# Performance work log

Measured on AMD Instinct MI355X. Metric: run time of the kernel, lower is better.

## Reference

```python
import jax, jax.numpy as jnp
import numpy as np

EPS_LN = 1e-5
EPS_D = 1e-8
K = 3

def layer_norm(x, g, b):
    mu = jnp.mean(x, axis=-1, keepdims=True)
    var = jnp.var(x, axis=-1, keepdims=True)
    return (x - mu) * jax.lax.rsqrt(var + EPS_LN) * g + b

def setup_inputs() -> dict:
    key = jax.random.key(0)
    ks = jax.random.split(key, 8)
    Nc, Nu, Cin, Cout = 4096, 16384, 256, 256
    return {
        "x_feat": jax.random.normal(ks[0], (Nc, Cin), jnp.float32),
        "x_pos": jax.random.uniform(ks[1], (Nc, 3), jnp.float32),
        "xup_feat": jax.random.normal(ks[2], (Nu, Cout), jnp.float32),
        "xup_pos": jax.random.uniform(ks[3], (Nu, 3), jnp.float32),
        "g1": jnp.ones((Cin,), jnp.float32),
        "b1": jnp.zeros((Cin,), jnp.float32),
        "W": jax.random.normal(ks[4], (Cin, Cout), jnp.float32) * 0.02,
        "b": jnp.zeros((Cout,), jnp.float32),
        "g2": jnp.ones((Cout,), jnp.float32),
        "b2": jnp.zeros((Cout,), jnp.float32),
        "W_up": jax.random.normal(ks[5], (Cout, Cout), jnp.float32) * 0.02,
        "b_up": jnp.zeros((Cout,), jnp.float32),
    }

def reference(x_feat, x_pos, xup_feat, xup_pos, g1, b1, W, b, g2, b2, W_up, b_up):
    # norm -> linear on coarse points: [Nc, Cout]
    x = layer_norm(x_feat, g1, b1) @ W + b
    # norm -> linear on fine points:   [Nu, Cout]
    xu = layer_norm(xup_feat, g2, b2) @ W_up + b_up
    # squared pairwise distances fine->coarse: [Nu, Nc]
    d2 = (jnp.sum(xup_pos * xup_pos, axis=-1, keepdims=True)
          - 2.0 * (xup_pos @ x_pos.T)
          + jnp.sum(x_pos * x_pos, axis=-1))
    # k nearest coarse neighbors per fine point
    neg_d2, idx = jax.lax.top_k(-d2, K)          # [Nu, K]
    w = 1.0 / (-neg_d2 + EPS_D)                  # inverse-distance weights
    w = w / jnp.sum(w, axis=-1, keepdims=True)
    # gather + weighted sum: [Nu, Cout]
    interp = jnp.einsum('uk,ukc->uc', w, x[idx])
    return interp + xu
```

## Files before the change

kernel.cpp:

```cpp
#include <hip/hip_runtime.h>

#define EPS_LN 1e-5f
#define EPS_D  1e-8f
#define BIGD 3.402823466e+38f

typedef __attribute__((ext_vector_type(8))) short s16x8;
typedef __attribute__((ext_vector_type(4))) float f32x4;
typedef __attribute__((ext_vector_type(4))) unsigned short u16x4;

#define XC_OFF    0u
#define XH_OFF    4194304u
#define XL_OFF    14680064u
#define MU_OFF    25165824u
#define RS_OFF    25247744u
#define WGH_OFF   25329664u
#define WGL_OFF   25460736u
#define WUGH_OFF  25591808u
#define WUGL_OFF  25722880u
#define C12_OFF   25853952u
#define CPS_OFF   25858048u
#define IDXS_OFF  25923584u
#define CST_OFF   25939968u
#define UPS_OFF   25944064u
#define USORT_OFF 26206208u

__device__ __forceinline__ int cell_of(float px, float py, float pz) {
    int cx = (int)(px * 8.0f); cx = cx < 0 ? 0 : (cx > 7 ? 7 : cx);
    int cy = (int)(py * 8.0f); cy = cy < 0 ? 0 : (cy > 7 ? 7 : cy);
    int cz = (int)(pz * 8.0f); cz = cz < 0 ? 0 : (cz > 7 ? 7 : cz);
    return (cz * 8 + cy) * 8 + cx;
}

__global__ __launch_bounds__(1024) void prep_kernel(
    const float* __restrict__ x_feat, const float* __restrict__ xup_feat,
    const float* __restrict__ x_pos, const float* __restrict__ xup_pos,
    const float* __restrict__ W, const float* __restrict__ W_up,
    const float* __restrict__ g1, const float* __restrict__ b1,
    const float* __restrict__ g2, const float* __restrict__ b2,
    float* __restrict__ mu, float* __restrict__ rs,
    unsigned short* __restrict__ xh, unsigned short* __restrict__ xl,
    unsigned short* __restrict__ wgh, unsigned short* __restrict__ wgl,
    unsigned short* __restrict__ wugh, unsigned short* __restrict__ wugl,
    float* __restrict__ c12,
    float4* __restrict__ cps, int* __restrict__ idxs, int* __restrict__ cellStart,
    float4* __restrict__ ups, int* __restrict__ usort)
{
    __shared__ float smemf[2048];
    int* const cnt   = (int*)smemf;
    int* const ofs   = ((int*)smemf) + 512;
    __shared__ int wpart[8];
    __shared__ int wpref[8];

    const int bid = blockIdx.x, tid = threadIdx.x;
    const int lane = tid & 63, wave = tid >> 6;

    if (bid < 2) {
        const bool fine = (bid == 0);
        const int npts = fine ? 16384 : 4096;
        const float* pos = fine ? xup_pos : x_pos;

        if (tid < 512) cnt[tid] = 0;
        __syncthreads();
        for (int i = tid; i < npts; i += 1024) {
            const int c = cell_of(pos[i*3+0], pos[i*3+1], pos[i*3+2]);
            atomicAdd(&cnt[c], 1);
        }
        __syncthreads();
        int v = 0, incl = 0;
        if (wave < 8) {
            const int cell = wave * 64 + lane;
            v = cnt[cell];
            incl = v;
            #pragma unroll
            for (int off = 1; off < 64; off <<= 1) {
                const int t = __shfl_up(incl, off);
                if (lane >= off) incl += t;
            }
            if (lane == 63) wpart[wave] = incl;
        }
        __syncthreads();
        if (tid == 0) {
            int run = 0;
            #pragma unroll
            for (int w = 0; w < 8; ++w) { wpref[w] = run; run += wpart[w]; }
        }
        __syncthreads();
        if (wave < 8) {
            const int cell = wave * 64 + lane;
            const int excl = incl - v + wpref[wave];
            ofs[cell] = excl;
            if (!fine) cellStart[cell] = excl;
        }
        if (!fine && tid == 0) cellStart[512] = 4096;
        __syncthreads();
        for (int i = tid; i < npts; i += 1024) {
            const float px = pos[i*3+0], py = pos[i*3+1], pz = pos[i*3+2];
            const int c = cell_of(px, py, pz);
            const int slot = atomicAdd(&ofs[c], 1);
            if (fine) {
                ups[slot] = make_float4(px, py, pz, px*px + py*py + pz*pz);
                usort[slot] = i;
            } else {
                cps[slot] = make_float4(px, py, pz, px*px + py*py + pz*pz);
                idxs[slot] = i;
            }
        }
    } else if (bid < 4) {
        const bool fine = (bid == 2);
        const float* src = fine ? W_up : W;
        const float* g   = fine ? g2 : g1;
        const float* bln = fine ? b2 : b1;
        float* c1 = c12 + (fine ? 0 : 512);
        float* c2 = c12 + (fine ? 256 : 768);
        const int col = tid & 255, kg = tid >> 8;
        float a1 = 0.0f, a2 = 0.0f;
        for (int k = kg * 64; k < kg * 64 + 64; ++k) {
            const float wv = src[(size_t)k * 256 + col];
            a1 = fmaf(bln[k], wv, a1);
            a2 = fmaf(g[k],   wv, a2);
        }
        smemf[kg * 256 + col] = a1;
        smemf[1024 + kg * 256 + col] = a2;
        __syncthreads();
        if (kg == 0) {
            c1[col] = smemf[col] + smemf[256 + col] + smemf[512 + col] + smemf[768 + col];
            c2[col] = smemf[1024 + col] + smemf[1280 + col] + smemf[1536 + col] + smemf[1792 + col];
        }
    } else if (bid < 8) {
        const int mb = (bid - 4) * 4 + (tid >> 8);
        const int t = tid & 255;
        const float* src = (mb < 8) ? W : W_up;
        const float* g   = (mb < 8) ? g1 : g2;
        unsigned short* dh = (mb < 8) ? wgh : wugh;
        unsigned short* dl = (mb < 8) ? wgl : wugl;
        const int n  = (mb & 7) * 32 + (t >> 3);
        const int kc = (t & 7) * 32;
        for (int kk = 0; kk < 32; kk += 4) {
            u16x4 hv, lv;
            #pragma unroll
            for (int c = 0; c < 4; ++c) {
                const int k = kc + kk + c;
                const float wv = g[k] * src[(size_t)k * 256 + n];
                const unsigned ua = __float_as_uint(wv);
                hv[c] = (unsigned short)(ua >> 16);
                const float lo = wv - __uint_as_float(ua & 0xFFFF0000u);
                lv[c] = (unsigned short)(__float_as_uint(lo) >> 16);
            }
            *(u16x4*)&dh[(size_t)n * 256 + kc + kk] = hv;
            *(u16x4*)&dl[(size_t)n * 256 + kc + kk] = lv;
        }
    } else {
        const int rbase = (bid - 8) * 128 + wave * 8;
        #pragma unroll
        for (int rr = 0; rr < 8; ++rr) {
            const int r = rbase + rr;
            const float* src = (r < 16384) ? (xup_feat + (size_t)r * 256)
                                           : (x_feat + (size_t)(r - 16384) * 256);
            const float4 v = ((const float4*)src)[lane];
            float s  = v.x + v.y + v.z + v.w;
            float ss = v.x*v.x + v.y*v.y + v.z*v.z + v.w*v.w;
            #pragma unroll
            for (int off = 1; off < 64; off <<= 1) {
                s  += __shfl_xor(s,  off);
                ss += __shfl_xor(ss, off);
            }
            if (lane == 0) {
                const float m   = s * (1.0f / 256.0f);
                const float var = ss * (1.0f / 256.0f) - m * m;
                mu[r] = m;
                rs[r] = rsqrtf(var + EPS_LN);
            }
            const float vv[4] = { v.x, v.y, v.z, v.w };
            u16x4 hv, lv;
            #pragma unroll
            for (int c = 0; c < 4; ++c) {
                const unsigned ua = __float_as_uint(vv[c]);
                hv[c] = (unsigned short)(ua >> 16);
                const float lo = vv[c] - __uint_as_float(ua & 0xFFFF0000u);
                lv[c] = (unsigned short)(__float_as_uint(lo) >> 16);
            }
            *(u16x4*)&xh[(size_t)r * 256 + lane * 4] = hv;
            *(u16x4*)&xl[(size_t)r * 256 + lane * 4] = lv;
        }
    }
}

__global__ __launch_bounds__(256) void gemm_kernel(
    const unsigned short* __restrict__ xh, const unsigned short* __restrict__ xl,
    const float* __restrict__ mu, const float* __restrict__ rs,
    const unsigned short* __restrict__ wgh, const unsigned short* __restrict__ wgl,
    const unsigned short* __restrict__ wugh, const unsigned short* __restrict__ wugl,
    const float* __restrict__ c12,
    const float* __restrict__ b_up, const float* __restrict__ bb,
    float* __restrict__ outF, float* __restrict__ outC)
{
    const int bid = blockIdx.x;
    const unsigned short *BH, *BL; const float *c1, *c2, *bias; float* OUT;
    int row0, col0, statbase;
    if (bid < 256) {
        BH = wugh; BL = wugl; c1 = c12; c2 = c12 + 256; bias = b_up; OUT = outF;
        row0 = (bid >> 1) * 128; col0 = (bid & 1) * 128; statbase = 0;
    } else {
        const int id = bid - 256;
        BH = wgh; BL = wgl; c1 = c12 + 512; c2 = c12 + 768; bias = bb; OUT = outC;
        row0 = (id >> 1) * 128; col0 = (id & 1) * 128; statbase = 16384;
    }

    const int lane = threadIdx.x & 63;
    const int wave = threadIdx.x >> 6;
    const int wr = wave >> 1, wc = wave & 1;
    const int lm = lane & 15, lk = lane >> 4;

    int arow[4];
    #pragma unroll
    for (int mf = 0; mf < 4; ++mf)
        arow[mf] = statbase + row0 + wr * 64 + mf * 16 + lm;

    int ncol[4]; float c1v[4], c2v[4], bv[4];
    #pragma unroll
    for (int nf = 0; nf < 4; ++nf) {
        ncol[nf] = col0 + wc * 64 + nf * 16 + lm;
        c1v[nf] = c1[ncol[nf]];
        c2v[nf] = c2[ncol[nf]];
        bv[nf]  = bias[ncol[nf]];
    }

    f32x4 acc[4][4];
    #pragma unroll
    for (int mf = 0; mf < 4; ++mf)
        #pragma unroll
        for (int nf = 0; nf < 4; ++nf)
            acc[mf][nf] = (f32x4){0.0f, 0.0f, 0.0f, 0.0f};

    for (int k0 = 0; k0 < 256; k0 += 32) {
        const int kb = k0 + lk * 8;

        s16x8 bh[4], bl[4], ah[4], al[4];
        #pragma unroll
        for (int nf = 0; nf < 4; ++nf) {
            const size_t o = (size_t)ncol[nf] * 256 + kb;
            bh[nf] = *(const s16x8*)(BH + o);
            bl[nf] = *(const s16x8*)(BL + o);
        }
        #pragma unroll
        for (int mf = 0; mf < 4; ++mf) {
            const size_t o = (size_t)arow[mf] * 256 + kb;
            ah[mf] = *(const s16x8*)(xh + o);
            al[mf] = *(const s16x8*)(xl + o);
        }

        #pragma unroll
        for (int mf = 0; mf < 4; ++mf)
            #pragma unroll
            for (int nf = 0; nf < 4; ++nf) {
                acc[mf][nf] = __builtin_amdgcn_mfma_f32_16x16x32_bf16(ah[mf], bh[nf], acc[mf][nf], 0, 0, 0);
                acc[mf][nf] = __builtin_amdgcn_mfma_f32_16x16x32_bf16(ah[mf], bl[nf], acc[mf][nf], 0, 0, 0);
                acc[mf][nf] = __builtin_amdgcn_mfma_f32_16x16x32_bf16(al[mf], bh[nf], acc[mf][nf], 0, 0, 0);
            }
    }

    #pragma unroll
    for (int mf = 0; mf < 4; ++mf) {
        #pragma unroll
        for (int q = 0; q < 4; ++q) {
            const int orow = row0 + wr * 64 + mf * 16 + lk * 4 + q;
            const float m = mu[statbase + orow];
            const float s = rs[statbase + orow];
            const float ms = -m * s;
            #pragma unroll
            for (int nf = 0; nf < 4; ++nf)
                OUT[(size_t)orow * 256 + ncol[nf]] =
                    fmaf(s, acc[mf][nf][q], fmaf(ms, c2v[nf], c1v[nf]) + bv[nf]);
        }
    }
}

__device__ __forceinline__ void ins3(float d, int p,
    float& b0, float& b1, float& b2, int& p0, int& p1, int& p2)
{
    const bool lt0 = d < b0, lt1 = d < b1, lt2 = d < b2;
    const float n1 = lt0 ? b0 : (lt1 ? d : b1);
    const int   q1 = lt0 ? p0 : (lt1 ? p : p1);
    const float n2 = lt1 ? b1 : (lt2 ? d : b2);
    const int   q2 = lt1 ? p1 : (lt2 ? p : p2);
    b0 = lt0 ? d : b0;  p0 = lt0 ? p : p0;
    b1 = n1; p1 = q1;
    b2 = n2; p2 = q2;
}

__global__ __launch_bounds__(256) void topk_kernel(
    const float4* __restrict__ cps, const int* __restrict__ idxs,
    const int* __restrict__ cellStart,
    const float4* __restrict__ ups, const int* __restrict__ usort,
    const float* __restrict__ xc, float* __restrict__ out)
{
    __shared__ float pd[4][64][3];
    __shared__ int   pp[4][64][3];
    __shared__ float wsel[64][3];
    __shared__ int   isel[64][3];
    __shared__ int   uor[64];
    __shared__ int   cst[513];

    const int tid = threadIdx.x, lane = tid & 63, wave = tid >> 6;
    const int su = blockIdx.x * 64 + lane;

    for (int i = tid; i < 513; i += 256) cst[i] = cellStart[i];

    const float4 up = ups[su];
    const float ux = up.x, uy = up.y, uz = up.z, uu = up.w;
    if (wave == 0) uor[lane] = usort[su];
    int cx = (int)(ux * 8.0f); cx = cx < 0 ? 0 : (cx > 7 ? 7 : cx);
    int cy = (int)(uy * 8.0f); cy = cy < 0 ? 0 : (cy > 7 ? 7 : cy);
    int cz = (int)(uz * 8.0f); cz = cz < 0 ? 0 : (cz > 7 ? 7 : cz);

    __syncthreads();

    float b0 = BIGD, b1 = BIGD, b2 = BIGD;
    int p0 = 0, p1 = 0, p2 = 0;

    for (int cc = wave; cc < 27; cc += 4) {
        const int nx = cx + (cc % 3) - 1;
        const int ny = cy + ((cc / 3) % 3) - 1;
        const int nz = cz + (cc / 9) - 1;
        if ((unsigned)nx > 7u || (unsigned)ny > 7u || (unsigned)nz > 7u) continue;
        const int cell = (nz * 8 + ny) * 8 + nx;
        const int s = cst[cell], e = cst[cell + 1];
        if (s >= e) continue;
        float4 c = cps[s];
        for (int p = s; p < e; ++p) {
            const float4 nxt = (p + 1 < e) ? cps[p + 1] : c;
            const float dot = ux * c.x + uy * c.y + uz * c.z;
            const float d = (uu - 2.0f * dot) + c.w;
            ins3(d, p, b0, b1, b2, p0, p1, p2);
            c = nxt;
        }
    }

    pd[wave][lane][0] = b0; pd[wave][lane][1] = b1; pd[wave][lane][2] = b2;
    pp[wave][lane][0] = p0; pp[wave][lane][1] = p1; pp[wave][lane][2] = p2;
    __syncthreads();

    if (wave == 0) {
        for (int w = 1; w < 4; ++w) {
            #pragma unroll
            for (int e = 0; e < 3; ++e)
                ins3(pd[w][lane][e], pp[w][lane][e], b0, b1, b2, p0, p1, p2);
        }

        const float h = 0.125f;
        float gmin = BIGD;
        if (cx > 0) gmin = fminf(gmin, ux - (float)(cx - 1) * h);
        if (cx < 7) gmin = fminf(gmin, (float)(cx + 2) * h - ux);
        if (cy > 0) gmin = fminf(gmin, uy - (float)(cy - 1) * h);
        if (cy < 7) gmin = fminf(gmin, (float)(cy + 2) * h - uy);
        if (cz > 0) gmin = fminf(gmin, uz - (float)(cz - 1) * h);
        if (cz < 7) gmin = fminf(gmin, (float)(cz + 2) * h - uz);

        if (b2 > gmin * gmin) {
            b0 = b1 = b2 = BIGD; p0 = p1 = p2 = 0;
            for (int p = 0; p < 4096; ++p) {
                const float4 c = cps[p];
                const float dot = ux * c.x + uy * c.y + uz * c.z;
                const float d = (uu - 2.0f * dot) + c.w;
                ins3(d, p, b0, b1, b2, p0, p1, p2);
            }
        }

        float w0 = 1.0f / (b0 + EPS_D);
        float w1 = 1.0f / (b1 + EPS_D);
        float w2 = 1.0f / (b2 + EPS_D);
        const float inv = 1.0f / (w0 + w1 + w2);
        wsel[lane][0] = w0 * inv; wsel[lane][1] = w1 * inv; wsel[lane][2] = w2 * inv;
        isel[lane][0] = idxs[p0]; isel[lane][1] = idxs[p1]; isel[lane][2] = idxs[p2];
    }
    __syncthreads();

    #pragma unroll
    for (int r = 0; r < 16; ++r) {
        const int ul = wave * 16 + r;
        const float w0 = wsel[ul][0], w1 = wsel[ul][1], w2 = wsel[ul][2];
        const int a0 = isel[ul][0], a1 = isel[ul][1], a2 = isel[ul][2];
        const float4 v0 = ((const float4*)(xc + (size_t)a0 * 256))[lane];
        const float4 v1 = ((const float4*)(xc + (size_t)a1 * 256))[lane];
        const float4 v2 = ((const float4*)(xc + (size_t)a2 * 256))[lane];
        float4* op = (float4*)(out + (size_t)uor[ul] * 256);
        float4 o = op[lane];
        o.x += w0 * v0.x + w1 * v1.x + w2 * v2.x;
        o.y += w0 * v0.y + w1 * v1.y + w2 * v2.y;
        o.z += w0 * v0.z + w1 * v1.z + w2 * v2.z;
        o.w += w0 * v0.w + w1 * v1.w + w2 * v2.w;
        op[lane] = o;
    }
}

extern "C" void kernel_launch(void* const* d_in, const int* in_sizes, int n_in,
                              void* d_out, int out_size, void* d_ws, size_t ws_size,
                              hipStream_t stream)
{
    const float* x_feat   = (const float*)d_in[0];
    const float* x_pos    = (const float*)d_in[1];
    const float* xup_feat = (const float*)d_in[2];
    const float* xup_pos  = (const float*)d_in[3];
    const float* g1       = (const float*)d_in[4];
    const float* b1       = (const float*)d_in[5];
    const float* W        = (const float*)d_in[6];
    const float* bb       = (const float*)d_in[7];
    const float* g2       = (const float*)d_in[8];
    const float* b2       = (const float*)d_in[9];
    const float* W_up     = (const float*)d_in[10];
    const float* b_up     = (const float*)d_in[11];

    float* out = (float*)d_out;
    char*  ws  = (char*)d_ws;

    float* xc  = (float*)(ws + XC_OFF);
    unsigned short* xh   = (unsigned short*)(ws + XH_OFF);
    unsigned short* xl   = (unsigned short*)(ws + XL_OFF);
    float* mu  = (float*)(ws + MU_OFF);
    float* rs  = (float*)(ws + RS_OFF);
    unsigned short* wgh  = (unsigned short*)(ws + WGH_OFF);
    unsigned short* wgl  = (unsigned short*)(ws + WGL_OFF);
    unsigned short* wugh = (unsigned short*)(ws + WUGH_OFF);
    unsigned short* wugl = (unsigned short*)(ws + WUGL_OFF);
    float* c12 = (float*)(ws + C12_OFF);
    float4* cps = (float4*)(ws + CPS_OFF);
    int* idxs   = (int*)(ws + IDXS_OFF);
    int* cstart = (int*)(ws + CST_OFF);
    float4* ups = (float4*)(ws + UPS_OFF);
    int* usort  = (int*)(ws + USORT_OFF);

    prep_kernel<<<168, 1024, 0, stream>>>(x_feat, xup_feat, x_pos, xup_pos,
                                          W, W_up, g1, b1, g2, b2,
                                          mu, rs, xh, xl,
                                          wgh, wgl, wugh, wugl,
                                          c12, cps, idxs, cstart, ups, usort);
    gemm_kernel<<<320, 256, 0, stream>>>(xh, xl, mu, rs,
                                         wgh, wgl, wugh, wugl,
                                         c12, b_up, bb, out, xc);
    topk_kernel<<<256, 256, 0, stream>>>(cps, idxs, cstart, ups, usort, xc, out);
}
```

Before: 180.5 us.

## Split prep and topk kernels; decouple kNN search from gather-interpolation

Splits the prep kernel into a small block for spatial-grid and weight prep and a streaming block for layer-norm stats and bf16 hi/lo splitting. Also splits the top-k kernel into a kNN kernel that writes weights and indices to workspace, and a separate interpolation kernel with more, smaller blocks. The kNN search now runs before the GEMM, so it no longer sits behind it. The cost is two extra launches, serialized on one stream, plus a round trip through global memory for the selected weights and indices.

```diff
diff --git a/kernel.cpp b/kernel.cpp
--- a/kernel.cpp
+++ b/kernel.cpp
@@ -23,6 +23,8 @@
 #define CST_OFF   25939968u
 #define UPS_OFF   25944064u
 #define USORT_OFF 26206208u
+#define WSEL_OFF  26271744u
+#define ISEL_OFF  26468352u
 
 __device__ __forceinline__ int cell_of(float px, float py, float pz) {
     int cx = (int)(px * 8.0f); cx = cx < 0 ? 0 : (cx > 7 ? 7 : cx);
@@ -31,14 +33,11 @@
     return (cz * 8 + cy) * 8 + cx;
 }
 
-__global__ __launch_bounds__(1024) void prep_kernel(
-    const float* __restrict__ x_feat, const float* __restrict__ xup_feat,
+__global__ __launch_bounds__(1024) void prep_small_kernel(
     const float* __restrict__ x_pos, const float* __restrict__ xup_pos,
     const float* __restrict__ W, const float* __restrict__ W_up,
     const float* __restrict__ g1, const float* __restrict__ b1,
     const float* __restrict__ g2, const float* __restrict__ b2,
-    float* __restrict__ mu, float* __restrict__ rs,
-    unsigned short* __restrict__ xh, unsigned short* __restrict__ xl,
     unsigned short* __restrict__ wgh, unsigned short* __restrict__ wgl,
     unsigned short* __restrict__ wugh, unsigned short* __restrict__ wugl,
     float* __restrict__ c12,
@@ -46,8 +45,8 @@
     float4* __restrict__ ups, int* __restrict__ usort)
 {
     __shared__ float smemf[2048];
-    int* const cnt   = (int*)smemf;
-    int* const ofs   = ((int*)smemf) + 512;
+    int* const cnt = (int*)smemf;
+    int* const ofs = ((int*)smemf) + 512;
     __shared__ int wpart[8];
     __shared__ int wpref[8];
 
@@ -126,7 +125,7 @@
             c1[col] = smemf[col] + smemf[256 + col] + smemf[512 + col] + smemf[768 + col];
             c2[col] = smemf[1024 + col] + smemf[1280 + col] + smemf[1536 + col] + smemf[1792 + col];
         }
-    } else if (bid < 8) {
+    } else {
         const int mb = (bid - 4) * 4 + (tid >> 8);
         const int t = tid & 255;
         const float* src = (mb < 8) ? W : W_up;
@@ -149,39 +148,46 @@
             *(u16x4*)&dh[(size_t)n * 256 + kc + kk] = hv;
             *(u16x4*)&dl[(size_t)n * 256 + kc + kk] = lv;
         }
-    } else {
-        const int rbase = (bid - 8) * 128 + wave * 8;
-        #pragma unroll
-        for (int rr = 0; rr < 8; ++rr) {
-            const int r = rbase + rr;
-            const float* src = (r < 16384) ? (xup_feat + (size_t)r * 256)
-                                           : (x_feat + (size_t)(r - 16384) * 256);
-            const float4 v = ((const float4*)src)[lane];
-            float s  = v.x + v.y + v.z + v.w;
-            float ss = v.x*v.x + v.y*v.y + v.z*v.z + v.w*v.w;
-            #pragma unroll
-            for (int off = 1; off < 64; off <<= 1) {
-                s  += __shfl_xor(s,  off);
-                ss += __shfl_xor(ss, off);
-            }
-            if (lane == 0) {
-                const float m   = s * (1.0f / 256.0f);
-                const float var = ss * (1.0f / 256.0f) - m * m;
-                mu[r] = m;
-                rs[r] = rsqrtf(var + EPS_LN);
-            }
-            const float vv[4] = { v.x, v.y, v.z, v.w };
-            u16x4 hv, lv;
-            #pragma unroll
-            for (int c = 0; c < 4; ++c) {
-                const unsigned ua = __float_as_uint(vv[c]);
-                hv[c] = (unsigned short)(ua >> 16);
-                const float lo = vv[c] - __uint_as_float(ua & 0xFFFF0000u);
-                lv[c] = (unsigned short)(__float_as_uint(lo) >> 16);
-            }
-            *(u16x4*)&xh[(size_t)r * 256 + lane * 4] = hv;
-            *(u16x4*)&xl[(size_t)r * 256 + lane * 4] = lv;
-        }
+    }
+}
+
+__global__ __launch_bounds__(1024) void prep_stream_kernel(
+    const float* __restrict__ x_feat, const float* __restrict__ xup_feat,
+    float* __restrict__ mu, float* __restrict__ rs,
+    unsigned short* __restrict__ xh, unsigned short* __restrict__ xl)
+{
+    const int lane = threadIdx.x & 63, wave = threadIdx.x >> 6;
+    const int rbase = blockIdx.x * 128 + wave * 8;
+    #pragma unroll
+    for (int rr = 0; rr < 8; ++rr) {
+        const int r = rbase + rr;
+        const float* src = (r < 16384) ? (xup_feat + (size_t)r * 256)
+                                       : (x_feat + (size_t)(r - 16384) * 256);
+        const float4 v = ((const float4*)src)[lane];
+        float s  = v.x + v.y + v.z + v.w;
+        float ss = v.x*v.x + v.y*v.y + v.z*v.z + v.w*v.w;
+        #pragma unroll
+        for (int off = 1; off < 64; off <<= 1) {
+            s  += __shfl_xor(s,  off);
+            ss += __shfl_xor(ss, off);
+        }
+        if (lane == 0) {
+            const float m   = s * (1.0f / 256.0f);
+            const float var = ss * (1.0f / 256.0f) - m * m;
+            mu[r] = m;
+            rs[r] = rsqrtf(var + EPS_LN);
+        }
+        const float vv[4] = { v.x, v.y, v.z, v.w };
+        u16x4 hv, lv;
+        #pragma unroll
+        for (int c = 0; c < 4; ++c) {
+            const unsigned ua = __float_as_uint(vv[c]);
+            hv[c] = (unsigned short)(ua >> 16);
+            const float lo = vv[c] - __uint_as_float(ua & 0xFFFF0000u);
+            lv[c] = (unsigned short)(__float_as_uint(lo) >> 16);
+        }
+        *(u16x4*)&xh[(size_t)r * 256 + lane * 4] = hv;
+        *(u16x4*)&xl[(size_t)r * 256 + lane * 4] = lv;
     }
 }
 
@@ -288,17 +294,14 @@
     b2 = n2; p2 = q2;
 }
 
-__global__ __launch_bounds__(256) void topk_kernel(
+__global__ __launch_bounds__(256) void knn_kernel(
     const float4* __restrict__ cps, const int* __restrict__ idxs,
     const int* __restrict__ cellStart,
-    const float4* __restrict__ ups, const int* __restrict__ usort,
-    const float* __restrict__ xc, float* __restrict__ out)
+    const float4* __restrict__ ups,
+    float* __restrict__ wsel, int* __restrict__ isel)
 {
     __shared__ float pd[4][64][3];
     __shared__ int   pp[4][64][3];
-    __shared__ float wsel[64][3];
-    __shared__ int   isel[64][3];
-    __shared__ int   uor[64];
     __shared__ int   cst[513];
 
     const int tid = threadIdx.x, lane = tid & 63, wave = tid >> 6;
@@ -308,7 +311,6 @@
 
     const float4 up = ups[su];
     const float ux = up.x, uy = up.y, uz = up.z, uu = up.w;
-    if (wave == 0) uor[lane] = usort[su];
     int cx = (int)(ux * 8.0f); cx = cx < 0 ? 0 : (cx > 7 ? 7 : cx);
     int cy = (int)(uy * 8.0f); cy = cy < 0 ? 0 : (cy > 7 ? 7 : cy);
     int cz = (int)(uz * 8.0f); cz = cz < 0 ? 0 : (cz > 7 ? 7 : cz);
@@ -370,20 +372,27 @@
         float w1 = 1.0f / (b1 + EPS_D);
         float w2 = 1.0f / (b2 + EPS_D);
         const float inv = 1.0f / (w0 + w1 + w2);
-        wsel[lane][0] = w0 * inv; wsel[lane][1] = w1 * inv; wsel[lane][2] = w2 * inv;
-        isel[lane][0] = idxs[p0]; isel[lane][1] = idxs[p1]; isel[lane][2] = idxs[p2];
-    }
-    __syncthreads();
-
-    #pragma unroll
-    for (int r = 0; r < 16; ++r) {
-        const int ul = wave * 16 + r;
-        const float w0 = wsel[ul][0], w1 = wsel[ul][1], w2 = wsel[ul][2];
-        const int a0 = isel[ul][0], a1 = isel[ul][1], a2 = isel[ul][2];
+        wsel[su*3+0] = w0 * inv; wsel[su*3+1] = w1 * inv; wsel[su*3+2] = w2 * inv;
+        isel[su*3+0] = idxs[p0]; isel[su*3+1] = idxs[p1]; isel[su*3+2] = idxs[p2];
+    }
+}
+
+__global__ __launch_bounds__(256) void interp_kernel(
+    const float* __restrict__ wsel, const int* __restrict__ isel,
+    const int* __restrict__ usort,
+    const float* __restrict__ xc, float* __restrict__ out)
+{
+    const int lane = threadIdx.x & 63, wave = threadIdx.x >> 6;
+    const int base = blockIdx.x * 32 + wave * 8;
+    #pragma unroll
+    for (int r = 0; r < 8; ++r) {
+        const int su = base + r;
+        const float w0 = wsel[su*3+0], w1 = wsel[su*3+1], w2 = wsel[su*3+2];
+        const int a0 = isel[su*3+0], a1 = isel[su*3+1], a2 = isel[su*3+2];
         const float4 v0 = ((const float4*)(xc + (size_t)a0 * 256))[lane];
         const float4 v1 = ((const float4*)(xc + (size_t)a1 * 256))[lane];
         const float4 v2 = ((const float4*)(xc + (size_t)a2 * 256))[lane];
-        float4* op = (float4*)(out + (size_t)uor[ul] * 256);
+        float4* op = (float4*)(out + (size_t)usort[su] * 256);
         float4 o = op[lane];
         o.x += w0 * v0.x + w1 * v1.x + w2 * v2.x;
         o.y += w0 * v0.y + w1 * v1.y + w2 * v2.y;
@@ -428,14 +437,17 @@
     int* cstart = (int*)(ws + CST_OFF);
     float4* ups = (float4*)(ws + UPS_OFF);
     int* usort  = (int*)(ws + USORT_OFF);
-
-    prep_kernel<<<168, 1024, 0, stream>>>(x_feat, xup_feat, x_pos, xup_pos,
-                                          W, W_up, g1, b1, g2, b2,
-                                          mu, rs, xh, xl,
-                                          wgh, wgl, wugh, wugl,
-                                          c12, cps, idxs, cstart, ups, usort);
+    float* wsel = (float*)(ws + WSEL_OFF);
+    int* isel   = (int*)(ws + ISEL_OFF);
+
+    prep_small_kernel<<<8, 1024, 0, stream>>>(x_pos, xup_pos, W, W_up,
+                                              g1, b1, g2, b2,
+                                              wgh, wgl, wugh, wugl,
+                                              c12, cps, idxs, cstart, ups, usort);
+    prep_stream_kernel<<<160, 1024, 0, stream>>>(x_feat, xup_feat, mu, rs, xh, xl);
+    knn_kernel<<<256, 256, 0, stream>>>(cps, idxs, cstart, ups, wsel, isel);
     gemm_kernel<<<320, 256, 0, stream>>>(xh, xl, mu, rs,
                                          wgh, wgl, wugh, wugl,
                                          c12, b_up, bb, out, xc);
-    topk_kernel<<<256, 256, 0, stream>>>(cps, idxs, cstart, ups, usort, xc, out);
-}
+    interp_kernel<<<512, 256, 0, stream>>>(wsel, isel, usort, xc, out);
+}
```

After: 189.1 us. 4.8% more time.
